# Kernel tuning notes

Measured on AMD Instinct MI355X. Metric: run time of the kernel, lower is better.

## Reference

```python
import jax, jax.numpy as jnp
import numpy as np

MODEL_DIM = 1024
NUM_HEADS = 16
HEAD_DIM = MODEL_DIM // NUM_HEADS
BATCH = 2
SEQ = 2048


def setup_inputs() -> dict:
    key = jax.random.key(0)
    k1, k2, k3 = jax.random.split(key, 3)
    scale = 1.0 / np.sqrt(MODEL_DIM)
    return {
        "embeddings": jax.random.normal(k1, (BATCH, SEQ, MODEL_DIM), dtype=jnp.float32),
        "w_qkv": jax.random.normal(k2, (MODEL_DIM, 3 * MODEL_DIM), dtype=jnp.float32) * scale,
        "b_qkv": jnp.zeros((3 * MODEL_DIM,), dtype=jnp.float32),
        "w_out": jax.random.normal(k3, (MODEL_DIM, MODEL_DIM), dtype=jnp.float32) * scale,
        "b_out": jnp.zeros((MODEL_DIM,), dtype=jnp.float32),
    }


def reference(embeddings, w_qkv, b_qkv, w_out, b_out):
    B, S, _ = embeddings.shape
    # fused QKV projection: [B, S, 3*model_dim]
    qkv = embeddings @ w_qkv + b_qkv
    # -> [B, H, S, 3*head_dim], then split
    qkv = qkv.reshape(B, S, NUM_HEADS, 3 * HEAD_DIM).transpose(0, 2, 1, 3)
    q, k, v = jnp.split(qkv, 3, axis=-1)
    # scaled dot-product attention (full O(S^2) matrix, as in original)
    scale = 1.0 / jnp.sqrt(jnp.asarray(HEAD_DIM, dtype=embeddings.dtype))
    scores = jnp.einsum("bhqd,bhkd->bhqk", q, k) * scale
    attn = jax.nn.softmax(scores, axis=-1)
    ctx = jnp.einsum("bhqk,bhkd->bhqd", attn, v)
    # merge heads -> [B, S, model_dim], output projection
    ctx = ctx.transpose(0, 2, 1, 3).reshape(B, S, NUM_HEADS * HEAD_DIM)
    return ctx @ w_out + b_out
```

## Files before the change

kernel.cpp:

```cpp
#include <hip/hip_runtime.h>
#include <hip/hip_bf16.h>

#define MODEL 1024
#define NHEADS 16
#define HDIM 64
#define BATCH 2
#define SEQ 2048
#define NROWS (BATCH*SEQ)
#define QKVN (3*MODEL)
#define QSCALE 0.1803368801111204f

typedef __bf16 bf16x8 __attribute__((ext_vector_type(8)));
typedef float f32x4 __attribute__((ext_vector_type(4)));
typedef float f32x16 __attribute__((ext_vector_type(16)));

#define GLDS(g, l) __builtin_amdgcn_global_load_lds( \
    (const __attribute__((address_space(1))) void*)(g), \
    (__attribute__((address_space(3))) void*)(l), 16, 0, 0)

__device__ inline unsigned cvtpk(float lo, float hi) {
    unsigned r;
    asm("v_cvt_pk_bf16_f32 %0, %1, %2" : "=v"(r) : "v"(lo), "v"(hi));
    return r;
}

__device__ inline int qk_fs(int s) { return ((s >> 6) << 12) + (((s >> 5) & 1) << 11) + ((s & 31) << 3); }
__device__ inline int qk_fd(int d) { return ((d >> 4) << 9) + (((d >> 3) & 1) << 8) + (d & 7); }
__device__ inline int v_fs(int s) { return ((s >> 6) << 12) + (((s >> 4) & 3) << 9) + (((s >> 3) & 1) << 8) + (s & 7); }
__device__ inline int v_fd(int d) { return ((d >> 5) << 11) + ((d & 31) << 3); }


__global__ __launch_bounds__(256) void prep_kernel(
    const float* __restrict__ emb, __hip_bfloat16* __restrict__ Xb,
    const float* __restrict__ wqkv, __hip_bfloat16* __restrict__ Wqkvt,
    const float* __restrict__ wout, __hip_bfloat16* __restrict__ Woutt)
{
    __shared__ float tile[32][33];
    int bid = blockIdx.x, tid = threadIdx.x;
    if (bid < 4096) {
        int i = (bid * 256 + tid) * 4;
        float4 v = *(const float4*)(emb + i);
        Xb[i + 0] = __float2bfloat16(v.x);
        Xb[i + 1] = __float2bfloat16(v.y);
        Xb[i + 2] = __float2bfloat16(v.z);
        Xb[i + 3] = __float2bfloat16(v.w);
        return;
    }
    const float* in; __hip_bfloat16* out; int K, N, n0, k0;
    if (bid < 7168) {
        int t = bid - 4096; in = wqkv; out = Wqkvt; K = MODEL; N = QKVN;
        n0 = (t % 96) * 32; k0 = (t / 96) * 32;
    } else {
        int t = bid - 7168; in = wout; out = Woutt; K = MODEL; N = MODEL;
        n0 = (t & 31) * 32; k0 = (t >> 5) * 32;
    }
    int tx = tid & 31, ty = tid >> 5;
#pragma unroll
    for (int i = 0; i < 4; ++i)
        tile[ty + i * 8][tx] = in[(size_t)(k0 + ty + i * 8) * N + n0 + tx];
    __syncthreads();
#pragma unroll
    for (int i = 0; i < 4; ++i)
        out[(size_t)(n0 + ty + i * 8) * K + k0 + tx] = __float2bfloat16(tile[tx][ty + i * 8]);
}


template<int EPI>
__global__ __launch_bounds__(256) void gemm_bt_kernel(
    const __hip_bfloat16* __restrict__ A, const __hip_bfloat16* __restrict__ Bt,
    const float* __restrict__ bias, float* __restrict__ Cf,
    __hip_bfloat16* __restrict__ qb, __hip_bfloat16* __restrict__ kb,
    __hip_bfloat16* __restrict__ vb, int M, int N, int K)
{
    __shared__ __hip_bfloat16 As[128 * 64];
    __shared__ __hip_bfloat16 Bs[128 * 64];
    int tid = threadIdx.x;
    int lane = tid & 63, wv = tid >> 6;
    int wm = wv >> 1, wn = wv & 1;
    int g = lane >> 4, li = lane & 15;
    int row0 = blockIdx.y * 128, col0 = blockIdx.x * 128;

    int cswz = ((tid & 7) ^ ((tid >> 3) & 7)) * 8;

    f32x4 acc[4][4] = {};

    for (int kt = 0; kt < K; kt += 64) {
        __syncthreads();
#pragma unroll
        for (int s4 = 0; s4 < 4; ++s4) {
            int r = s4 * 32 + (tid >> 3);
            GLDS(A + (size_t)(row0 + r) * K + kt + cswz, (char*)As + (size_t)(s4 * 4 + wv) * 1024);
            GLDS(Bt + (size_t)(col0 + r) * K + kt + cswz, (char*)Bs + (size_t)(s4 * 4 + wv) * 1024);
        }
        __syncthreads();
        bf16x8 a[2][4], b[2][4];
#pragma unroll
        for (int kk = 0; kk < 2; ++kk) {
#pragma unroll
            for (int m = 0; m < 4; ++m) {
                int row = wm * 64 + m * 16 + li;
                a[kk][m] = *(const bf16x8*)((const char*)As + row * 128 + (((kk * 4 + g) ^ (li & 7)) << 4));
            }
#pragma unroll
            for (int n = 0; n < 4; ++n) {
                int row = wn * 64 + n * 16 + li;
                b[kk][n] = *(const bf16x8*)((const char*)Bs + row * 128 + (((kk * 4 + g) ^ (li & 7)) << 4));
            }
        }
#pragma unroll
        for (int m = 0; m < 4; ++m)
#pragma unroll
            for (int n = 0; n < 4; ++n) {
                acc[m][n] = __builtin_amdgcn_mfma_f32_16x16x32_bf16(a[0][m], b[0][n], acc[m][n], 0, 0, 0);
                acc[m][n] = __builtin_amdgcn_mfma_f32_16x16x32_bf16(a[1][m], b[1][n], acc[m][n], 0, 0, 0);
            }
    }

    if (EPI == 1) {
#pragma unroll
        for (int m = 0; m < 4; ++m) {
            int row = row0 + wm * 64 + m * 16 + g * 4;
#pragma unroll
            for (int n = 0; n < 4; ++n) {
                int col = col0 + wn * 64 + n * 16 + li;
                float bv = bias[col];
#pragma unroll
                for (int r = 0; r < 4; ++r)
                    Cf[(size_t)(row + r) * N + col] = acc[m][n][r] + bv;
            }
        }
    } else {
        __hip_bfloat16* dstn[4];
        float bvn[4], qmn[4];
        int tpn[4];
#pragma unroll
        for (int n = 0; n < 4; ++n) {
            int col = col0 + wn * 64 + n * 16 + li;
            int h = col / 192;
            int rem = col - h * 192;
            int t = rem >> 6, d = rem & 63;
            tpn[n] = t;
            qmn[n] = (t == 0) ? QSCALE : 1.0f;
            bvn[n] = bias[col];
            __hip_bfloat16* base = (t == 0) ? qb : ((t == 1) ? kb : vb);
            dstn[n] = base + (size_t)h * (SEQ * HDIM) + ((t == 2) ? v_fd(d) : qk_fd(d));
        }
#pragma unroll
        for (int m = 0; m < 4; ++m)
#pragma unroll
            for (int r = 0; r < 4; ++r) {
                int row = row0 + wm * 64 + m * 16 + g * 4 + r;
                int s = row & 2047;
                int bofs = (row >> 11) * (NHEADS * SEQ * HDIM);
                int fsqk = qk_fs(s), fsv = v_fs(s);
#pragma unroll
                for (int n = 0; n < 4; ++n) {
                    float val = (acc[m][n][r] + bvn[n]) * qmn[n];
                    int off = bofs + ((tpn[n] == 2) ? fsv : fsqk);
                    dstn[n][off] = __float2bfloat16(val);
                }
            }
    }
}


__global__ __launch_bounds__(256, 4) void attn_kernel(
    const __hip_bfloat16* __restrict__ qfb, const __hip_bfloat16* __restrict__ kfb,
    const __hip_bfloat16* __restrict__ vfb, __hip_bfloat16* __restrict__ ctx)
{
    __shared__ float Ms[2][64], Ls[2][64], Os[2][32][64];
    int tid = threadIdx.x;
    int lane = tid & 63, w = tid >> 6;
    int qg = w & 1, kvh = w >> 1;
    int qi = lane & 31, hi = lane >> 5;
    int bh = blockIdx.x;
    int b = bh >> 4, h = bh & 15;
    int q0 = blockIdx.y * 64 + qg * 32;

    const bf16x8* QF = (const bf16x8*)qfb + (size_t)bh * 16384;
    const bf16x8* KF = (const bf16x8*)kfb + (size_t)bh * 16384;
    const bf16x8* VF = (const bf16x8*)vfb + (size_t)bh * 16384;

    bf16x8 qv[4];
#pragma unroll
    for (int st = 0; st < 4; ++st)
        qv[st] = QF[(size_t)blockIdx.y * 512 + (qg * 4 + st) * 64 + lane];

    f32x16 o0 = {}, o1 = {};
    float m = -INFINITY, l = 0.f;

    bf16x8 kc[4], kn[4];
    {
        int t32 = kvh * 32, t64 = t32 >> 1, rh = t32 & 1;
#pragma unroll
        for (int st = 0; st < 4; ++st)
            kc[st] = KF[(size_t)t64 * 512 + (rh * 4 + st) * 64 + lane];
    }

    for (int tt = 0; tt < 32; ++tt) {
        int t32 = kvh * 32 + tt;
        int t64 = t32 >> 1, rh = t32 & 1;
        __builtin_amdgcn_s_barrier();

        f32x16 s = {};
#pragma unroll
        for (int st = 0; st < 4; ++st)
            s = __builtin_amdgcn_mfma_f32_32x32x16_bf16(kc[st], qv[st], s, 0, 0, 0);

        bf16x8 vv[4];
#pragma unroll
        for (int dr = 0; dr < 2; ++dr)
#pragma unroll
            for (int ksl = 0; ksl < 2; ++ksl)
                vv[dr * 2 + ksl] = VF[(size_t)t64 * 512 + (dr * 4 + rh * 2 + ksl) * 64 + lane];
        {
            int tp = (tt < 31) ? t32 + 1 : t32;
            int p64 = tp >> 1, ph = tp & 1;
#pragma unroll
            for (int st = 0; st < 4; ++st)
                kn[st] = KF[(size_t)p64 * 512 + (ph * 4 + st) * 64 + lane];
        }

        float tm[8];
#pragma unroll
        for (int i = 0; i < 8; ++i) tm[i] = fmaxf(s[i], s[8 + i]);
#pragma unroll
        for (int i = 0; i < 4; ++i) tm[i] = fmaxf(tm[i], tm[4 + i]);
        float mx = fmaxf(fmaxf(tm[0], tm[1]), fmaxf(tm[2], tm[3]));
        mx = fmaxf(mx, __shfl_xor(mx, 32));
        if (__any(mx - m > 8.0f)) {
            float mn = fmaxf(m, mx);
            float al = __builtin_amdgcn_exp2f(m - mn);
            m = mn;
            l *= al;
#pragma unroll
            for (int i = 0; i < 16; ++i) { o0[i] *= al; o1[i] *= al; }
        }
#pragma unroll
        for (int i = 0; i < 16; ++i) s[i] = __builtin_amdgcn_exp2f(s[i] - m);
        float ts[8];
#pragma unroll
        for (int i = 0; i < 8; ++i) ts[i] = s[i] + s[8 + i];
#pragma unroll
        for (int i = 0; i < 4; ++i) ts[i] = ts[i] + ts[4 + i];
        float sum = (ts[0] + ts[1]) + (ts[2] + ts[3]);
        l += sum;

        bf16x8 pb[2];
#pragma unroll
        for (int ksl = 0; ksl < 2; ++ksl) {
            const int base = ksl * 8;
            unsigned t0 = cvtpk(s[base + 0], s[base + 1]);
            unsigned t1 = cvtpk(s[base + 2], s[base + 3]);
            unsigned u0 = cvtpk(s[base + 4], s[base + 5]);
            unsigned u1 = cvtpk(s[base + 6], s[base + 7]);
            unsigned ra = __shfl_xor(hi ? t0 : u0, 32);
            unsigned rb = __shfl_xor(hi ? t1 : u1, 32);
            union { unsigned u[4]; bf16x8 v; } pk;
            pk.u[0] = hi ? ra : t0;
            pk.u[1] = hi ? rb : t1;
            pk.u[2] = hi ? u0 : ra;
            pk.u[3] = hi ? u1 : rb;
            pb[ksl] = pk.v;
        }

        o0 = __builtin_amdgcn_mfma_f32_32x32x16_bf16(vv[0], pb[0], o0, 0, 0, 0);
        o0 = __builtin_amdgcn_mfma_f32_32x32x16_bf16(vv[1], pb[1], o0, 0, 0, 0);
        o1 = __builtin_amdgcn_mfma_f32_32x32x16_bf16(vv[2], pb[0], o1, 0, 0, 0);
        o1 = __builtin_amdgcn_mfma_f32_32x32x16_bf16(vv[3], pb[1], o1, 0, 0, 0);

#pragma unroll
        for (int st = 0; st < 4; ++st) kc[st] = kn[st];
    }

    l += __shfl_xor(l, 32);

    __syncthreads();
    if (kvh == 1) {
        Ms[qg][lane] = m; Ls[qg][lane] = l;
#pragma unroll
        for (int i = 0; i < 16; ++i) { Os[qg][i][lane] = o0[i]; Os[qg][16 + i][lane] = o1[i]; }
    }
    __syncthreads();
    if (kvh == 0) {
        float m2 = Ms[qg][lane], l2 = Ls[qg][lane];
        float mn = fmaxf(m, m2);
        float a = __builtin_amdgcn_exp2f(m - mn);
        float b2 = __builtin_amdgcn_exp2f(m2 - mn);
        float linv = 1.f / (l * a + l2 * b2);
        __hip_bfloat16* crow = ctx + ((size_t)(b * SEQ) + q0 + qi) * MODEL + h * HDIM;
#pragma unroll
        for (int rg = 0; rg < 4; ++rg) {
            float c0[4], c1[4];
#pragma unroll
            for (int e = 0; e < 4; ++e) {
                int i = rg * 4 + e;
                c0[e] = (o0[i] * a + Os[qg][i][lane] * b2) * linv;
                c1[e] = (o1[i] * a + Os[qg][16 + i][lane] * b2) * linv;
            }
            uint2 pk0, pk1;
            pk0.x = cvtpk(c0[0], c0[1]); pk0.y = cvtpk(c0[2], c0[3]);
            pk1.x = cvtpk(c1[0], c1[1]); pk1.y = cvtpk(c1[2], c1[3]);
            *(uint2*)(crow + rg * 8 + hi * 4) = pk0;
            *(uint2*)(crow + 32 + rg * 8 + hi * 4) = pk1;
        }
    }
}


extern "C" void kernel_launch(void* const* d_in, const int* in_sizes, int n_in,
                              void* d_out, int out_size, void* d_ws, size_t ws_size,
                              hipStream_t stream) {
    const float* emb = (const float*)d_in[0];
    const float* w_qkv = (const float*)d_in[1];
    const float* b_qkv = (const float*)d_in[2];
    const float* w_out = (const float*)d_in[3];
    const float* b_out = (const float*)d_in[4];
    float* out = (float*)d_out;
    char* ws = (char*)d_ws;

    __hip_bfloat16* Xb    = (__hip_bfloat16*)(ws);
    __hip_bfloat16* Wqkvt = (__hip_bfloat16*)(ws + ((size_t)8  << 20));
    __hip_bfloat16* Woutt = (__hip_bfloat16*)(ws + ((size_t)14 << 20));
    __hip_bfloat16* qbuf  = (__hip_bfloat16*)(ws + ((size_t)16 << 20));
    __hip_bfloat16* kbuf  = (__hip_bfloat16*)(ws + ((size_t)24 << 20));
    __hip_bfloat16* vbuf  = (__hip_bfloat16*)(ws + ((size_t)32 << 20));
    __hip_bfloat16* ctx   = (__hip_bfloat16*)(ws + ((size_t)40 << 20));

    prep_kernel<<<8192, 256, 0, stream>>>(emb, Xb, w_qkv, Wqkvt, w_out, Woutt);

    gemm_bt_kernel<0><<<dim3(QKVN / 128, NROWS / 128), 256, 0, stream>>>(
        Xb, Wqkvt, b_qkv, nullptr, qbuf, kbuf, vbuf, NROWS, QKVN, MODEL);

    attn_kernel<<<dim3(BATCH * NHEADS, SEQ / 64), 256, 0, stream>>>(qbuf, kbuf, vbuf, ctx);

    gemm_bt_kernel<1><<<dim3(MODEL / 128, NROWS / 128), 256, 0, stream>>>(
        ctx, Woutt, b_out, out, nullptr, nullptr, nullptr, NROWS, MODEL, MODEL);
}
```

Baseline: 203.0 us.

## Swizzle block order for XCD locality and streamline attention softmax inner loop

Remaps block IDs in both GEMMs and in the attention kernel so that consecutive blocks dispatched round-robin across the 8 XCDs work on the same tiles or heads, improving L2 reuse. In attention it also drops the per-iteration s_barrier, computes the row max with v_max3_f32, and replaces the shuffle-plus-select exchange of packed P values with v_permlane32_swap. The swizzle assumes the grid size divides evenly by 8, and removing the barrier lets waves drift apart, which may change cache sharing between them.

```diff
diff --git a/kernel.cpp b/kernel.cpp
--- a/kernel.cpp
+++ b/kernel.cpp
@@ -21,6 +21,12 @@
 __device__ inline unsigned cvtpk(float lo, float hi) {
     unsigned r;
     asm("v_cvt_pk_bf16_f32 %0, %1, %2" : "=v"(r) : "v"(lo), "v"(hi));
+    return r;
+}
+
+__device__ inline float max3f(float a, float b, float c) {
+    float r;
+    asm("v_max3_f32 %0, %1, %2, %3" : "=v"(r) : "v"(a), "v"(b), "v"(c));
     return r;
 }
 
@@ -78,7 +84,12 @@
     int lane = tid & 63, wv = tid >> 6;
     int wm = wv >> 1, wn = wv & 1;
     int g = lane >> 4, li = lane & 15;
-    int row0 = blockIdx.y * 128, col0 = blockIdx.x * 128;
+
+    int nbx = gridDim.x;
+    int flat = blockIdx.y * nbx + blockIdx.x;
+    int chunk = (nbx * gridDim.y) >> 3;
+    int swz = (flat & 7) * chunk + (flat >> 3);
+    int row0 = (swz / nbx) * 128, col0 = (swz % nbx) * 128;
 
     int cswz = ((tid & 7) ^ ((tid >> 3) & 7)) * 8;
 
@@ -173,9 +184,12 @@
     int lane = tid & 63, w = tid >> 6;
     int qg = w & 1, kvh = w >> 1;
     int qi = lane & 31, hi = lane >> 5;
-    int bh = blockIdx.x;
+
+    int bid = blockIdx.y * 32 + blockIdx.x;
+    int swz = (bid & 7) * 128 + (bid >> 3);
+    int bh = swz >> 5, qt = swz & 31;
     int b = bh >> 4, h = bh & 15;
-    int q0 = blockIdx.y * 64 + qg * 32;
+    int q0 = qt * 64 + qg * 32;
 
     const bf16x8* QF = (const bf16x8*)qfb + (size_t)bh * 16384;
     const bf16x8* KF = (const bf16x8*)kfb + (size_t)bh * 16384;
@@ -184,7 +198,7 @@
     bf16x8 qv[4];
 #pragma unroll
     for (int st = 0; st < 4; ++st)
-        qv[st] = QF[(size_t)blockIdx.y * 512 + (qg * 4 + st) * 64 + lane];
+        qv[st] = QF[(size_t)qt * 512 + (qg * 4 + st) * 64 + lane];
 
     f32x16 o0 = {}, o1 = {};
     float m = -INFINITY, l = 0.f;
@@ -200,7 +214,6 @@
     for (int tt = 0; tt < 32; ++tt) {
         int t32 = kvh * 32 + tt;
         int t64 = t32 >> 1, rh = t32 & 1;
-        __builtin_amdgcn_s_barrier();
 
         f32x16 s = {};
 #pragma unroll
@@ -221,12 +234,12 @@
                 kn[st] = KF[(size_t)p64 * 512 + (ph * 4 + st) * 64 + lane];
         }
 
-        float tm[8];
-#pragma unroll
-        for (int i = 0; i < 8; ++i) tm[i] = fmaxf(s[i], s[8 + i]);
-#pragma unroll
-        for (int i = 0; i < 4; ++i) tm[i] = fmaxf(tm[i], tm[4 + i]);
-        float mx = fmaxf(fmaxf(tm[0], tm[1]), fmaxf(tm[2], tm[3]));
+        float t0m = max3f(s[0], s[1], s[2]);
+        float t1m = max3f(s[3], s[4], s[5]);
+        float t2m = max3f(s[6], s[7], s[8]);
+        float t3m = max3f(s[9], s[10], s[11]);
+        float t4m = max3f(s[12], s[13], s[14]);
+        float mx = fmaxf(max3f(t0m, t1m, t2m), max3f(t3m, t4m, s[15]));
         mx = fmaxf(mx, __shfl_xor(mx, 32));
         if (__any(mx - m > 8.0f)) {
             float mn = fmaxf(m, mx);
@@ -250,17 +263,17 @@
 #pragma unroll
         for (int ksl = 0; ksl < 2; ++ksl) {
             const int base = ksl * 8;
-            unsigned t0 = cvtpk(s[base + 0], s[base + 1]);
-            unsigned t1 = cvtpk(s[base + 2], s[base + 3]);
-            unsigned u0 = cvtpk(s[base + 4], s[base + 5]);
-            unsigned u1 = cvtpk(s[base + 6], s[base + 7]);
-            unsigned ra = __shfl_xor(hi ? t0 : u0, 32);
-            unsigned rb = __shfl_xor(hi ? t1 : u1, 32);
+            unsigned w0 = cvtpk(s[base + 0], s[base + 1]);
+            unsigned w1 = cvtpk(s[base + 2], s[base + 3]);
+            unsigned w2 = cvtpk(s[base + 4], s[base + 5]);
+            unsigned w3 = cvtpk(s[base + 6], s[base + 7]);
+            asm("v_permlane32_swap_b32 %0, %1" : "+v"(w0), "+v"(w2));
+            asm("v_permlane32_swap_b32 %0, %1" : "+v"(w1), "+v"(w3));
             union { unsigned u[4]; bf16x8 v; } pk;
-            pk.u[0] = hi ? ra : t0;
-            pk.u[1] = hi ? rb : t1;
-            pk.u[2] = hi ? u0 : ra;
-            pk.u[3] = hi ? u1 : rb;
+            pk.u[0] = w0;
+            pk.u[1] = w1;
+            pk.u[2] = w2;
+            pk.u[3] = w3;
             pb[ksl] = pk.v;
         }
 
@@ -332,7 +345,7 @@
     gemm_bt_kernel<0><<<dim3(QKVN / 128, NROWS / 128), 256, 0, stream>>>(
         Xb, Wqkvt, b_qkv, nullptr, qbuf, kbuf, vbuf, NROWS, QKVN, MODEL);
 
-    attn_kernel<<<dim3(BATCH * NHEADS, SEQ / 64), 256, 0, stream>>>(qbuf, kbuf, vbuf, ctx);
+    attn_kernel<<<dim3(32, 32), 256, 0, stream>>>(qbuf, kbuf, vbuf, ctx);
 
     gemm_bt_kernel<1><<<dim3(MODEL / 128, NROWS / 128), 256, 0, stream>>>(
         ctx, Woutt, b_out, out, nullptr, nullptr, nullptr, NROWS, MODEL, MODEL);
```

Measured after the change: 198.6 us. -2.1%, faster.
